# Kernel tuning notes

Hardware: AMD Instinct MI355X
Metric: run time of the kernel (lower is better)

Reference implementation:

```python
import jax, jax.numpy as jnp
import numpy as np

B, T, C = 1, 4096, 1024
H = 16
D = C // H  # 64
LN_EPS = 1e-5


def layer_norm(x, g, b):
    mu = jnp.mean(x, axis=-1, keepdims=True)
    var = jnp.mean(jnp.square(x - mu), axis=-1, keepdims=True)
    return (x - mu) * jax.lax.rsqrt(var + LN_EPS) * g + b


def setup_inputs() -> dict:
    key = jax.random.key(0)
    ks = jax.random.split(key, 8)
    s = 0.02
    return {
        "x": jax.random.normal(ks[0], (B, T, C), dtype=jnp.float32),
        "ln1_g": jnp.ones((C,), jnp.float32),
        "ln1_b": jnp.zeros((C,), jnp.float32),
        "Wqkv": jax.random.normal(ks[1], (C, 3 * C), dtype=jnp.float32) * s,
        "bqkv": jnp.zeros((3 * C,), jnp.float32),
        "Wo": jax.random.normal(ks[2], (C, C), dtype=jnp.float32) * s,
        "bo": jnp.zeros((C,), jnp.float32),
        "ln2_g": jnp.ones((C,), jnp.float32),
        "ln2_b": jnp.zeros((C,), jnp.float32),
        "W1": jax.random.normal(ks[3], (C, 4 * C), dtype=jnp.float32) * s,
        "b1": jnp.zeros((4 * C,), jnp.float32),
        "W2": jax.random.normal(ks[4], (4 * C, C), dtype=jnp.float32) * s,
        "b2": jnp.zeros((C,), jnp.float32),
    }


def reference(x, ln1_g, ln1_b, Wqkv, bqkv, Wo, bo, ln2_g, ln2_b, W1, b1, W2, b2):
    b, t, c = x.shape
    x_norm = layer_norm(x, ln1_g, ln1_b)
    qkv = x_norm @ Wqkv + bqkv                      # [B,T,3C]
    qkv = qkv.reshape(b, t, 3, H, D).transpose(2, 0, 3, 1, 4)  # [3,B,H,T,D]
    Q, K, V = qkv[0], qkv[1], qkv[2]
    scores = jnp.einsum("bhtd,bhsd->bhts", Q, K) / jnp.sqrt(jnp.float32(D))
    causal = jnp.tril(jnp.ones((t, t), dtype=bool))  # [T,T]
    scores = jnp.where(causal[None, None], scores, -jnp.inf)
    weights = jax.nn.softmax(scores, axis=-1)
    attn = jnp.einsum("bhts,bhsd->bhtd", weights, V)  # [B,H,T,D]
    attn = attn.transpose(0, 2, 1, 3).reshape(b, t, c)
    x = x + (attn @ Wo + bo)
    h = layer_norm(x, ln2_g, ln2_b)
    h = jax.nn.gelu(h @ W1 + b1, approximate=False) @ W2 + b2
    return x + h
```

## Files before the change

kernel.cpp:

```cpp
#include <hip/hip_runtime.h>
#include <math.h>

typedef __bf16 bf16_t;
typedef __attribute__((ext_vector_type(8))) __bf16 bf16x8;
typedef __attribute__((ext_vector_type(4))) __bf16 bf16x4;
typedef __attribute__((ext_vector_type(4))) float f32x4;
typedef __attribute__((ext_vector_type(16))) float f32x16;
typedef __attribute__((ext_vector_type(4))) unsigned int u32x4;

#define T_LEN 4096
#define C_DIM 1024
#define NH 16
#define HD 64

__device__ __forceinline__ void gload_lds16(const void* g, void* l) {
    __builtin_amdgcn_global_load_lds(
        (__attribute__((address_space(1))) void*)(g),
        (__attribute__((address_space(3))) void*)(l), 16, 0, 0);
}

__device__ __forceinline__ f32x4 mfma16(bf16x8 a, bf16x8 b, f32x4 c) {
    return __builtin_amdgcn_mfma_f32_16x16x32_bf16(a, b, c, 0, 0, 0);
}

__device__ __forceinline__ f32x16 mfma32(bf16x8 a, bf16x8 b, f32x16 c) {
    return __builtin_amdgcn_mfma_f32_32x32x16_bf16(a, b, c, 0, 0, 0);
}

__device__ __forceinline__ float gelu_exact(float v) {
    return 0.5f * v * (1.0f + erff(v * 0.7071067811865476f));
}

__device__ __forceinline__ void make_frags2(const f32x16 s, bf16x8& fx, bf16x8& fy) {
    unsigned a0, a1, b0, b1;
    asm("v_cvt_pk_bf16_f32 %0, %1, %2" : "=v"(a0) : "v"(s[0]), "v"(s[1]));
    asm("v_cvt_pk_bf16_f32 %0, %1, %2" : "=v"(a1) : "v"(s[2]), "v"(s[3]));
    asm("v_cvt_pk_bf16_f32 %0, %1, %2" : "=v"(b0) : "v"(s[4]), "v"(s[5]));
    asm("v_cvt_pk_bf16_f32 %0, %1, %2" : "=v"(b1) : "v"(s[6]), "v"(s[7]));
    asm("v_permlane32_swap_b32 %0, %1" : "+v"(a0), "+v"(b0));
    asm("v_permlane32_swap_b32 %0, %1" : "+v"(a1), "+v"(b1));
    u32x4 wa = {a0, a1, b0, b1};
    fx = __builtin_bit_cast(bf16x8, wa);
    unsigned c0, c1, d0, d1;
    asm("v_cvt_pk_bf16_f32 %0, %1, %2" : "=v"(c0) : "v"(s[8]), "v"(s[9]));
    asm("v_cvt_pk_bf16_f32 %0, %1, %2" : "=v"(c1) : "v"(s[10]), "v"(s[11]));
    asm("v_cvt_pk_bf16_f32 %0, %1, %2" : "=v"(d0) : "v"(s[12]), "v"(s[13]));
    asm("v_cvt_pk_bf16_f32 %0, %1, %2" : "=v"(d1) : "v"(s[14]), "v"(s[15]));
    asm("v_permlane32_swap_b32 %0, %1" : "+v"(c0), "+v"(d0));
    asm("v_permlane32_swap_b32 %0, %1" : "+v"(c1), "+v"(d1));
    u32x4 wb = {c0, c1, d0, d1};
    fy = __builtin_bit_cast(bf16x8, wb);
}

__global__ __launch_bounds__(256) void transpose_w(
    const float* __restrict__ in, bf16_t* __restrict__ out, int R, int C)
{
    __shared__ float tile[32][33];
    const int tx = threadIdx.x, ty = threadIdx.y;
    const int c0 = blockIdx.x * 32, r0 = blockIdx.y * 32;
#pragma unroll
    for (int j = 0; j < 4; ++j)
        tile[ty + j * 8][tx] = in[(size_t)(r0 + ty + j * 8) * C + c0 + tx];
    __syncthreads();
#pragma unroll
    for (int j = 0; j < 4; ++j)
        out[(size_t)(c0 + ty + j * 8) * R + r0 + tx] = (bf16_t)tile[tx][ty + j * 8];
}

__global__ __launch_bounds__(256) void vtrans(
    const bf16_t* __restrict__ qkv, bf16_t* __restrict__ vt)
{
    __shared__ bf16_t tile[32][33];
    const int tx = threadIdx.x, ty = threadIdx.y;
    const int h = blockIdx.z;
    const int t0 = blockIdx.x * 32, d0 = blockIdx.y * 32;
#pragma unroll
    for (int j = 0; j < 4; ++j)
        tile[ty + j * 8][tx] =
            qkv[(size_t)(t0 + ty + j * 8) * 3072 + 2048 + h * 64 + d0 + tx];
    __syncthreads();
#pragma unroll
    for (int j = 0; j < 4; ++j)
        vt[(size_t)h * (64 * 4096) + (size_t)(d0 + ty + j * 8) * 4096 + t0 + tx] =
            tile[tx][ty + j * 8];
}

__global__ __launch_bounds__(256) void ln_bf16(
    const float* __restrict__ x, const float* __restrict__ gam,
    const float* __restrict__ bet, bf16_t* __restrict__ out)
{
    const int row = blockIdx.x, t = threadIdx.x;
    const float4 v = *(const float4*)(x + (size_t)row * 1024 + t * 4);
    float s1 = v.x + v.y + v.z + v.w;
    float s2 = v.x * v.x + v.y * v.y + v.z * v.z + v.w * v.w;
#pragma unroll
    for (int m = 1; m < 64; m <<= 1) {
        s1 += __shfl_xor(s1, m);
        s2 += __shfl_xor(s2, m);
    }
    __shared__ float red[8];
    if ((t & 63) == 0) { red[(t >> 6) * 2] = s1; red[(t >> 6) * 2 + 1] = s2; }
    __syncthreads();
    s1 = red[0] + red[2] + red[4] + red[6];
    s2 = red[1] + red[3] + red[5] + red[7];
    const float mu = s1 * (1.0f / 1024.0f);
    const float inv = rsqrtf(s2 * (1.0f / 1024.0f) - mu * mu + 1e-5f);
    const float4 gg = *(const float4*)(gam + t * 4);
    const float4 bb = *(const float4*)(bet + t * 4);
    bf16x4 o;
    o[0] = (bf16_t)((v.x - mu) * inv * gg.x + bb.x);
    o[1] = (bf16_t)((v.y - mu) * inv * gg.y + bb.y);
    o[2] = (bf16_t)((v.z - mu) * inv * gg.z + bb.z);
    o[3] = (bf16_t)((v.w - mu) * inv * gg.w + bb.w);
    *(bf16x4*)(out + (size_t)row * 1024 + t * 4) = o;
}

template <int EPI>
__global__ __launch_bounds__(256, 2) void gemm_bt(
    const bf16_t* __restrict__ A, const bf16_t* __restrict__ Bt,
    const float* __restrict__ bias, const float* __restrict__ res,
    bf16_t* __restrict__ outb, float* __restrict__ outf,
    int M, int N, int K)
{
    __shared__ alignas(1024) bf16_t Alds[4][128 * 32];
    __shared__ alignas(1024) bf16_t Blds[4][128 * 32];
    const int t = threadIdx.x;
    const int lane = t & 63, w = t >> 6;
    const int wr = w >> 1, wc = w & 1;
    const int g = lane >> 4, ci = lane & 15;

    const int NB = gridDim.x, MB = gridDim.y;
    const int flat = blockIdx.x + NB * blockIdx.y;
    const int xcd = flat & 7, slot = flat >> 3;
    const int by = xcd * (MB >> 3) + slot / NB;
    const int bx = slot % NB;
    const int m0 = by * 128, n0 = bx * 128;

    f32x4 acc[4][4];
#pragma unroll
    for (int i = 0; i < 4; ++i)
#pragma unroll
        for (int j = 0; j < 4; ++j)
#pragma unroll
            for (int k = 0; k < 4; ++k) acc[i][j][k] = 0.0f;

    const int r0 = t >> 2;
    const int cc = (t & 3) * 8;
    const int nkt = K >> 5;

    auto stage = [&](int kt) {
        const int b = kt & 3;
        const int kk = kt * 32;
        char* aB = (char*)&Alds[b][0] + w * 1024;
        char* bB = (char*)&Blds[b][0] + w * 1024;
        gload_lds16(A + (size_t)(m0 + r0) * K + kk + cc, aB);
        gload_lds16(A + (size_t)(m0 + r0 + 64) * K + kk + cc, aB + 4096);
        gload_lds16(Bt + (size_t)(n0 + r0) * K + kk + cc, bB);
        gload_lds16(Bt + (size_t)(n0 + r0 + 64) * K + kk + cc, bB + 4096);
    };

    stage(0);
    if (nkt > 1) stage(1);
    for (int kt = 0; kt < nkt; ++kt) {
        if (kt + 2 < nkt) {
            stage(kt + 2);
            asm volatile("s_waitcnt vmcnt(8)" ::: "memory");
        } else if (kt + 1 < nkt) {
            asm volatile("s_waitcnt vmcnt(4)" ::: "memory");
        } else {
            asm volatile("s_waitcnt vmcnt(0)" ::: "memory");
        }
        __builtin_amdgcn_s_barrier();
        __builtin_amdgcn_sched_barrier(0);
        const int b = kt & 3;
        const bf16_t* ap = &Alds[b][0] + (wr * 64 + ci) * 32 + g * 8;
        const bf16_t* bp = &Blds[b][0] + (wc * 64 + ci) * 32 + g * 8;
        bf16x8 af[4], bf[4];
#pragma unroll
        for (int mt = 0; mt < 4; ++mt) af[mt] = *(const bf16x8*)(ap + mt * 16 * 32);
#pragma unroll
        for (int nt = 0; nt < 4; ++nt) bf[nt] = *(const bf16x8*)(bp + nt * 16 * 32);
        __builtin_amdgcn_s_setprio(1);
#pragma unroll
        for (int mt = 0; mt < 4; ++mt)
#pragma unroll
            for (int nt = 0; nt < 4; ++nt)
                acc[mt][nt] = mfma16(af[mt], bf[nt], acc[mt][nt]);
        __builtin_amdgcn_s_setprio(0);
    }

#pragma unroll
    for (int nt = 0; nt < 4; ++nt) {
        const int col = n0 + wc * 64 + nt * 16 + ci;
        const float bv = bias[col];
#pragma unroll
        for (int mt = 0; mt < 4; ++mt) {
            const int row = m0 + wr * 64 + mt * 16 + g * 4;
#pragma unroll
            for (int r = 0; r < 4; ++r) {
                float v = acc[mt][nt][r] + bv;
                if constexpr (EPI == 1) v = gelu_exact(v);
                if constexpr (EPI == 2) {
                    outf[(size_t)(row + r) * N + col] =
                        v + res[(size_t)(row + r) * N + col];
                } else {
                    outb[(size_t)(row + r) * N + col] = (bf16_t)v;
                }
            }
        }
    }
}

template <int EPI>
__global__ __launch_bounds__(512, 2) void gemm256(
    const bf16_t* __restrict__ A, const bf16_t* __restrict__ Bt,
    const float* __restrict__ bias, bf16_t* __restrict__ outb,
    int M, int N, int K)
{
    __shared__ alignas(1024) bf16_t lds[2][2][256 * 64];
    const int t = threadIdx.x, lane = t & 63, w = t >> 6;
    const int g = lane >> 4, ci = lane & 15;
    const int wr = w >> 2, wc = w & 3;
    const int m0 = blockIdx.y * 256, n0 = blockIdx.x * 256;
    const int NKT = K >> 6;

    f32x4 acc[8][4];
#pragma unroll
    for (int i = 0; i < 8; ++i)
#pragma unroll
        for (int j = 0; j < 4; ++j)
#pragma unroll
            for (int k2 = 0; k2 < 4; ++k2) acc[i][j][k2] = 0.0f;

    const int sw0 = (g ^ (ci & 7)) * 8;
    const int sw1 = ((4 + g) ^ (ci & 7)) * 8;

    auto stage = [&](int h, int ktile, int b) {
#pragma unroll
        for (int i = 0; i < 2; ++i) {
            const int idx = i * 512 + t;
            const int r = idx >> 3;
            const int c = (t & 7) ^ (r & 7);
            const bf16_t* src = ((h < 2) ? A : Bt)
                + (size_t)(((h < 2) ? m0 : n0) + (h & 1) * 128 + r) * K
                + ktile * 64 + c * 8;
            bf16_t* dst = &lds[b][h >> 1][(h & 1) * 8192] + (i * 512 + w * 64) * 8;
            gload_lds16(src, dst);
        }
    };

    bf16x8 a[4][2], b2[2][2][2];

    stage(0, 0, 0); stage(3, 0, 0); stage(1, 0, 0); stage(2, 0, 0);
    if (NKT > 1) { stage(0, 1, 1); stage(3, 1, 1); stage(1, 1, 1); }
    asm volatile("s_waitcnt vmcnt(6)" ::: "memory");
    __builtin_amdgcn_s_barrier();

    for (int kt = 0; kt < NKT; ++kt) {
        const int cur = kt & 1;
        const bf16_t* Ab = &lds[cur][0][0];
        const bf16_t* Bb = &lds[cur][1][0];

#pragma unroll
        for (int mi = 0; mi < 4; ++mi) {
            const bf16_t* ap = Ab + (wr * 64 + mi * 16 + ci) * 64;
            a[mi][0] = *(const bf16x8*)(ap + sw0);
            a[mi][1] = *(const bf16x8*)(ap + sw1);
        }
#pragma unroll
        for (int ni = 0; ni < 2; ++ni) {
            const bf16_t* bp = Bb + (wc * 32 + ni * 16 + ci) * 64;
            b2[0][ni][0] = *(const bf16x8*)(bp + sw0);
            b2[0][ni][1] = *(const bf16x8*)(bp + sw1);
        }
        if (kt + 1 < NKT) stage(2, kt + 1, cur ^ 1);
        __builtin_amdgcn_s_barrier();
        asm volatile("s_waitcnt lgkmcnt(0)" ::: "memory");
        __builtin_amdgcn_sched_barrier(0);
        __builtin_amdgcn_s_setprio(1);
#pragma unroll
        for (int mi = 0; mi < 4; ++mi)
#pragma unroll
            for (int ni = 0; ni < 2; ++ni) {
                acc[mi][ni] = mfma16(a[mi][0], b2[0][ni][0], acc[mi][ni]);
                acc[mi][ni] = mfma16(a[mi][1], b2[0][ni][1], acc[mi][ni]);
            }
        __builtin_amdgcn_s_setprio(0);
        __builtin_amdgcn_s_barrier();

#pragma unroll
        for (int ni = 0; ni < 2; ++ni) {
            const bf16_t* bp = Bb + (128 + wc * 32 + ni * 16 + ci) * 64;
            b2[1][ni][0] = *(const bf16x8*)(bp + sw0);
            b2[1][ni][1] = *(const bf16x8*)(bp + sw1);
        }
        if (kt + 2 < NKT) stage(0, kt + 2, cur);
        __builtin_amdgcn_s_barrier();
        asm volatile("s_waitcnt lgkmcnt(0)" ::: "memory");
        __builtin_amdgcn_sched_barrier(0);
        __builtin_amdgcn_s_setprio(1);
#pragma unroll
        for (int mi = 0; mi < 4; ++mi)
#pragma unroll
            for (int ni = 0; ni < 2; ++ni) {
                acc[mi][2 + ni] = mfma16(a[mi][0], b2[1][ni][0], acc[mi][2 + ni]);
                acc[mi][2 + ni] = mfma16(a[mi][1], b2[1][ni][1], acc[mi][2 + ni]);
            }
        __builtin_amdgcn_s_setprio(0);
        __builtin_amdgcn_s_barrier();

#pragma unroll
        for (int mi = 0; mi < 4; ++mi) {
            const bf16_t* ap = Ab + (128 + wr * 64 + mi * 16 + ci) * 64;
            a[mi][0] = *(const bf16x8*)(ap + sw0);
            a[mi][1] = *(const bf16x8*)(ap + sw1);
        }
        if (kt + 2 < NKT) stage(3, kt + 2, cur);
        __builtin_amdgcn_s_barrier();
        asm volatile("s_waitcnt lgkmcnt(0)" ::: "memory");
        __builtin_amdgcn_sched_barrier(0);
        __builtin_amdgcn_s_setprio(1);
#pragma unroll
        for (int mi = 0; mi < 4; ++mi)
#pragma unroll
            for (int ni = 0; ni < 2; ++ni) {
                acc[4 + mi][2 + ni] = mfma16(a[mi][0], b2[1][ni][0], acc[4 + mi][2 + ni]);
                acc[4 + mi][2 + ni] = mfma16(a[mi][1], b2[1][ni][1], acc[4 + mi][2 + ni]);
            }
        __builtin_amdgcn_s_setprio(0);
        __builtin_amdgcn_s_barrier();

        if (kt + 2 < NKT) stage(1, kt + 2, cur);
        __builtin_amdgcn_s_barrier();
        __builtin_amdgcn_s_setprio(1);
#pragma unroll
        for (int mi = 0; mi < 4; ++mi)
#pragma unroll
            for (int ni = 0; ni < 2; ++ni) {
                acc[4 + mi][ni] = mfma16(a[mi][0], b2[0][ni][0], acc[4 + mi][ni]);
                acc[4 + mi][ni] = mfma16(a[mi][1], b2[0][ni][1], acc[4 + mi][ni]);
            }
        __builtin_amdgcn_s_setprio(0);
        if (kt + 2 < NKT) asm volatile("s_waitcnt vmcnt(6)" ::: "memory");
        else              asm volatile("s_waitcnt vmcnt(0)" ::: "memory");
        __builtin_amdgcn_s_barrier();
    }

#pragma unroll
    for (int mrep = 0; mrep < 8; ++mrep) {
        const int row = m0 + (mrep >> 2) * 128 + wr * 64 + (mrep & 3) * 16 + g * 4;
#pragma unroll
        for (int nrep = 0; nrep < 4; ++nrep) {
            const int col = n0 + (nrep >> 1) * 128 + wc * 32 + (nrep & 1) * 16 + ci;
            const float bv = bias[col];
#pragma unroll
            for (int jr = 0; jr < 4; ++jr) {
                float v = acc[mrep][nrep][jr] + bv;
                if constexpr (EPI == 1) v = gelu_exact(v);
                outb[(size_t)(row + jr) * N + col] = (bf16_t)v;
            }
        }
    }
}

__global__ __launch_bounds__(256, 2) void attn_fwd(
    const bf16_t* __restrict__ qkv, const bf16_t* __restrict__ vt,
    float* __restrict__ opart, float* __restrict__ mlbuf)
{
    __shared__ alignas(1024) bf16_t Klds[2][64 * 64];
    __shared__ alignas(1024) bf16_t Vlds[2][64 * 64];
    const int t = threadIdx.x, lane = t & 63, w = t >> 6;
    const int hi = lane >> 5, li = lane & 31;
    const int lq = li >> 2;
    const int h = blockIdx.x;
    const int y = blockIdx.y;
    const int qt = 31 - (y >> 1);
    const int chunk = y & 1;
    const int q0 = qt * 128;
    const int qrow = q0 + w * 32 + li;
    const int wDiag = 2 * qt + (w >> 1);
    const int ktA = chunk ? (qt + 1) : 0;
    const int ktB = chunk ? (2 * qt + 2) : (qt + 1);
    const float C1 = 0.125f * 1.4426950408889634f;

    bf16x8 qf[4];
#pragma unroll
    for (int ks = 0; ks < 4; ++ks)
        qf[ks] = *(const bf16x8*)(qkv + (size_t)qrow * 3072 + h * 64 + ks * 16 + hi * 8);

    f32x16 oacc[2];
#pragma unroll
    for (int d = 0; d < 2; ++d)
#pragma unroll
        for (int r = 0; r < 16; ++r) oacc[d][r] = 0.0f;
    float m_i = -1e30f, l_i = 0.0f;

    const int sr = t >> 3;
    const int sx = ((t & 7) ^ ((sr >> 2) & 7)) * 8;

    auto stageKV = [&](int kt, int b) {
        const size_t kbase = (size_t)(kt * 64) * 3072 + 1024 + h * 64 + sx;
        const size_t vbase = (size_t)h * 262144 + (size_t)kt * 64 + sx;
#pragma unroll
        for (int i = 0; i < 2; ++i) {
            gload_lds16(qkv + kbase + (size_t)(i * 32 + sr) * 3072,
                        (char*)&Klds[b][0] + (size_t)(i * 2048 + t * 8) * 2);
            gload_lds16(vt + vbase + (size_t)(i * 32 + sr) * 4096,
                        (char*)&Vlds[b][0] + (size_t)(i * 2048 + t * 8) * 2);
        }
    };

    stageKV(ktA, 0);
    for (int kt = ktA; kt < ktB; ++kt) {
        const int cur = (kt - ktA) & 1;
        asm volatile("s_waitcnt vmcnt(0)" ::: "memory");
        __syncthreads();
        if (kt + 1 < ktB) stageKV(kt + 1, cur ^ 1);

        if (kt <= wDiag) {
            const bf16_t* Kb = &Klds[cur][0];
            const bf16_t* Vb = &Vlds[cur][0];
            f32x16 s0, s1;
#pragma unroll
            for (int r = 0; r < 16; ++r) { s0[r] = 0.0f; s1[r] = 0.0f; }

            __builtin_amdgcn_s_setprio(1);
#pragma unroll
            for (int ks = 0; ks < 4; ++ks) {
                const int cs = ((ks * 2 + hi) ^ lq) * 8;
                s0 = mfma32(*(const bf16x8*)(Kb + li * 64 + cs), qf[ks], s0);
                s1 = mfma32(*(const bf16x8*)(Kb + (32 + li) * 64 + cs), qf[ks], s1);
            }
            __builtin_amdgcn_s_setprio(0);

            bf16x8 vf[4][2];
#pragma unroll
            for (int ks = 0; ks < 4; ++ks) {
                const int cs = ((ks * 2 + hi) ^ lq) * 8;
                vf[ks][0] = *(const bf16x8*)(Vb + li * 64 + cs);
                vf[ks][1] = *(const bf16x8*)(Vb + (32 + li) * 64 + cs);
            }

            if (kt == wDiag) {
                const int kb0 = kt * 64 + 4 * hi;
#pragma unroll
                for (int r = 0; r < 16; ++r) {
                    const int kp0 = kb0 + (r & 3) + 8 * (r >> 2);
                    if (kp0 > qrow) s0[r] = -1e30f;
                    if (kp0 + 32 > qrow) s1[r] = -1e30f;
                }
            }
            float mt8[8];
#pragma unroll
            for (int r = 0; r < 8; ++r)
                mt8[r] = fmaxf(fmaxf(s0[r], s0[r + 8]), fmaxf(s1[r], s1[r + 8]));
#pragma unroll
            for (int d = 4; d >= 1; d >>= 1)
#pragma unroll
                for (int r = 0; r < d; ++r) mt8[r] = fmaxf(mt8[r], mt8[r + d]);
            float mx = fmaxf(mt8[0], __shfl_xor(mt8[0], 32));
            const float pmax = mx * C1;
            if (!__all(pmax - m_i <= 8.0f)) {
                const float newm = fmaxf(m_i, pmax);
                const float scf = exp2f(m_i - newm);
                m_i = newm;
                l_i *= scf;
#pragma unroll
                for (int r = 0; r < 16; ++r) { oacc[0][r] *= scf; oacc[1][r] *= scf; }
            }
            float st8[8];
#pragma unroll
            for (int r = 0; r < 16; ++r) {
                s0[r] = exp2f(fmaf(s0[r], C1, -m_i));
                s1[r] = exp2f(fmaf(s1[r], C1, -m_i));
            }
#pragma unroll
            for (int r = 0; r < 8; ++r)
                st8[r] = (s0[r] + s0[r + 8]) + (s1[r] + s1[r + 8]);
#pragma unroll
            for (int d = 4; d >= 1; d >>= 1)
#pragma unroll
                for (int r = 0; r < d; ++r) st8[r] += st8[r + d];
            l_i += st8[0] + __shfl_xor(st8[0], 32);

            bf16x8 pf[4];
            make_frags2(s0, pf[0], pf[1]);
            make_frags2(s1, pf[2], pf[3]);

            __builtin_amdgcn_s_setprio(1);
#pragma unroll
            for (int ks = 0; ks < 4; ++ks) {
                oacc[0] = mfma32(vf[ks][0], pf[ks], oacc[0]);
                oacc[1] = mfma32(vf[ks][1], pf[ks], oacc[1]);
            }
            __builtin_amdgcn_s_setprio(0);
        }
        __syncthreads();
    }

    float* op = opart + ((size_t)chunk * T_LEN + qrow) * 1024 + h * 64 + hi * 4;
#pragma unroll
    for (int dblk = 0; dblk < 2; ++dblk)
#pragma unroll
        for (int gi = 0; gi < 4; ++gi) {
            f32x4 o4;
#pragma unroll
            for (int j = 0; j < 4; ++j) o4[j] = oacc[dblk][gi * 4 + j];
            *(f32x4*)(op + dblk * 32 + gi * 8) = o4;
        }
    if (hi == 0) {
        float2 ml = make_float2(m_i, l_i);
        *(float2*)(mlbuf + (((size_t)chunk * T_LEN + qrow) * NH + h) * 2) = ml;
    }
}

__global__ __launch_bounds__(256) void attn_combine(
    const float* __restrict__ opart, const float* __restrict__ mlbuf,
    bf16_t* __restrict__ out)
{
    const int row = blockIdx.x, t = threadIdx.x;
    const int c = t * 4, h = c >> 6;
    const float2 ml0 = *(const float2*)(mlbuf + ((size_t)row * NH + h) * 2);
    const float2 ml1 = *(const float2*)(mlbuf + (((size_t)T_LEN + row) * NH + h) * 2);
    const float M = fmaxf(ml0.x, ml1.x);
    const float w0 = exp2f(ml0.x - M), w1 = exp2f(ml1.x - M);
    const float inv = 1.0f / (ml0.y * w0 + ml1.y * w1);
    const float4 o0 = *(const float4*)(opart + (size_t)row * 1024 + c);
    const float4 o1 = *(const float4*)(opart + ((size_t)T_LEN + row) * 1024 + c);
    bf16x4 o;
    o[0] = (bf16_t)((o0.x * w0 + o1.x * w1) * inv);
    o[1] = (bf16_t)((o0.y * w0 + o1.y * w1) * inv);
    o[2] = (bf16_t)((o0.z * w0 + o1.z * w1) * inv);
    o[3] = (bf16_t)((o0.w * w0 + o1.w * w1) * inv);
    *(bf16x4*)(out + (size_t)row * 1024 + c) = o;
}

extern "C" void kernel_launch(void* const* d_in, const int* in_sizes, int n_in,
                              void* d_out, int out_size, void* d_ws, size_t ws_size,
                              hipStream_t stream)
{
    const float* x    = (const float*)d_in[0];
    const float* ln1g = (const float*)d_in[1];
    const float* ln1b = (const float*)d_in[2];
    const float* Wqkv = (const float*)d_in[3];
    const float* bqkv = (const float*)d_in[4];
    const float* Wo   = (const float*)d_in[5];
    const float* bo   = (const float*)d_in[6];
    const float* ln2g = (const float*)d_in[7];
    const float* ln2b = (const float*)d_in[8];
    const float* W1   = (const float*)d_in[9];
    const float* b1   = (const float*)d_in[10];
    const float* W2   = (const float*)d_in[11];
    const float* b2   = (const float*)d_in[12];
    float* outp = (float*)d_out;

    char* p = (char*)d_ws;
    bf16_t* WqkvT = (bf16_t*)p; p += (size_t)3072 * 1024 * 2;
    bf16_t* WoT   = (bf16_t*)p; p += (size_t)1024 * 1024 * 2;
    bf16_t* W1T   = (bf16_t*)p; p += (size_t)4096 * 1024 * 2;
    bf16_t* W2T   = (bf16_t*)p; p += (size_t)1024 * 4096 * 2;
    bf16_t* xn    = (bf16_t*)p; p += (size_t)4096 * 1024 * 2;
    bf16_t* qkv   = (bf16_t*)p; p += (size_t)4096 * 3072 * 2;
    bf16_t* vtb   = (bf16_t*)p; p += (size_t)16 * 64 * 4096 * 2;
    bf16_t* attnb = (bf16_t*)p; p += (size_t)4096 * 1024 * 2;
    float*  x2    = (float*)p;  p += (size_t)4096 * 1024 * 4;
    bf16_t* hb    = (bf16_t*)p; p += (size_t)4096 * 1024 * 2;
    bf16_t* g1    = (bf16_t*)p; p += (size_t)4096 * 4096 * 2;
    float*  opart = (float*)p;  p += (size_t)2 * 4096 * 1024 * 4;
    float*  mlbuf = (float*)p;  p += (size_t)2 * 4096 * 16 * 2 * 4;

    const dim3 tb(32, 8);
    transpose_w<<<dim3(96, 32),  tb, 0, stream>>>(Wqkv, WqkvT, 1024, 3072);
    transpose_w<<<dim3(32, 32),  tb, 0, stream>>>(Wo,   WoT,   1024, 1024);
    transpose_w<<<dim3(128, 32), tb, 0, stream>>>(W1,   W1T,   1024, 4096);
    transpose_w<<<dim3(32, 128), tb, 0, stream>>>(W2,   W2T,   4096, 1024);

    ln_bf16<<<4096, 256, 0, stream>>>(x, ln1g, ln1b, xn);
    gemm256<0><<<dim3(12, 16), 512, 0, stream>>>(xn, WqkvT, bqkv,
                                                 qkv, 4096, 3072, 1024);
    vtrans<<<dim3(128, 2, 16), tb, 0, stream>>>(qkv, vtb);
    attn_fwd<<<dim3(16, 64), 256, 0, stream>>>(qkv, vtb, opart, mlbuf);
    attn_combine<<<4096, 256, 0, stream>>>(opart, mlbuf, attnb);
    gemm_bt<2><<<dim3(8, 32), 256, 0, stream>>>(attnb, WoT, bo, x,
                                                nullptr, x2, 4096, 1024, 1024);
    ln_bf16<<<4096, 256, 0, stream>>>(x2, ln2g, ln2b, hb);
    gemm256<1><<<dim3(16, 16), 512, 0, stream>>>(hb, W1T, b1,
                                                 g1, 4096, 4096, 1024);
    gemm_bt<2><<<dim3(8, 32), 256, 0, stream>>>(g1, W2T, b2, x2,
                                                nullptr, outp, 4096, 1024, 4096);
}
```

Before: 286.5 us.

## Split-K the W2 GEMM into two chunks and remap gemm256 tiles across XCDs

The final W2 GEMM (K=4096) is split into two K-halves, launched as 512 blocks instead of 256, each writing fp32 partials into the reused attention partial buffer. A new combine kernel sums both partials and adds the bias and the residual. This aims to fill more CUs, since 256 blocks of 128x128 tiles underfill the device, at the cost of extra fp32 partial traffic and one more launch. gemm256 also gets an XCD-aware block-index remap intended to improve L2 locality.

```diff
diff --git a/kernel.cpp b/kernel.cpp
--- a/kernel.cpp
+++ b/kernel.cpp
@@ -120,7 +120,7 @@
     const bf16_t* __restrict__ A, const bf16_t* __restrict__ Bt,
     const float* __restrict__ bias, const float* __restrict__ res,
     bf16_t* __restrict__ outb, float* __restrict__ outf,
-    int M, int N, int K)
+    int M, int N, int Klen, int Kstr)
 {
     __shared__ alignas(1024) bf16_t Alds[4][128 * 32];
     __shared__ alignas(1024) bf16_t Blds[4][128 * 32];
@@ -129,11 +129,23 @@
     const int wr = w >> 1, wc = w & 1;
     const int g = lane >> 4, ci = lane & 15;
 
-    const int NB = gridDim.x, MB = gridDim.y;
-    const int flat = blockIdx.x + NB * blockIdx.y;
-    const int xcd = flat & 7, slot = flat >> 3;
-    const int by = xcd * (MB >> 3) + slot / NB;
-    const int bx = slot % NB;
+    int bx, by, chunk = 0;
+    if constexpr (EPI == 3) {
+        const int flat = blockIdx.x + 8 * blockIdx.y;
+        const int xcd = flat & 7, s = flat >> 3;
+        chunk = s >> 5;
+        const int s2 = s & 31;
+        by = xcd * 4 + (s2 >> 3);
+        bx = s2 & 7;
+        A  += (size_t)chunk * Klen;
+        Bt += (size_t)chunk * Klen;
+    } else {
+        const int NB = gridDim.x, MB = gridDim.y;
+        const int flat = blockIdx.x + NB * blockIdx.y;
+        const int xcd = flat & 7, slot = flat >> 3;
+        by = xcd * (MB >> 3) + slot / NB;
+        bx = slot % NB;
+    }
     const int m0 = by * 128, n0 = bx * 128;
 
     f32x4 acc[4][4];
@@ -146,17 +158,17 @@
 
     const int r0 = t >> 2;
     const int cc = (t & 3) * 8;
-    const int nkt = K >> 5;
+    const int nkt = Klen >> 5;
 
     auto stage = [&](int kt) {
         const int b = kt & 3;
         const int kk = kt * 32;
         char* aB = (char*)&Alds[b][0] + w * 1024;
         char* bB = (char*)&Blds[b][0] + w * 1024;
-        gload_lds16(A + (size_t)(m0 + r0) * K + kk + cc, aB);
-        gload_lds16(A + (size_t)(m0 + r0 + 64) * K + kk + cc, aB + 4096);
-        gload_lds16(Bt + (size_t)(n0 + r0) * K + kk + cc, bB);
-        gload_lds16(Bt + (size_t)(n0 + r0 + 64) * K + kk + cc, bB + 4096);
+        gload_lds16(A + (size_t)(m0 + r0) * Kstr + kk + cc, aB);
+        gload_lds16(A + (size_t)(m0 + r0 + 64) * Kstr + kk + cc, aB + 4096);
+        gload_lds16(Bt + (size_t)(n0 + r0) * Kstr + kk + cc, bB);
+        gload_lds16(Bt + (size_t)(n0 + r0 + 64) * Kstr + kk + cc, bB + 4096);
     };
 
     stage(0);
@@ -192,7 +204,7 @@
 #pragma unroll
     for (int nt = 0; nt < 4; ++nt) {
         const int col = n0 + wc * 64 + nt * 16 + ci;
-        const float bv = bias[col];
+        const float bv = (EPI == 3) ? 0.0f : bias[col];
 #pragma unroll
         for (int mt = 0; mt < 4; ++mt) {
             const int row = m0 + wr * 64 + mt * 16 + g * 4;
@@ -203,12 +215,32 @@
                 if constexpr (EPI == 2) {
                     outf[(size_t)(row + r) * N + col] =
                         v + res[(size_t)(row + r) * N + col];
+                } else if constexpr (EPI == 3) {
+                    outf[((size_t)chunk * M + row + r) * N + col] = v;
                 } else {
                     outb[(size_t)(row + r) * N + col] = (bf16_t)v;
                 }
             }
         }
     }
+}
+
+__global__ __launch_bounds__(256) void w2_combine(
+    const float* __restrict__ part, const float* __restrict__ bias,
+    const float* __restrict__ res, float* __restrict__ out)
+{
+    const int row = blockIdx.x, t = threadIdx.x;
+    const int c = t * 4;
+    const float4 a = *(const float4*)(part + (size_t)row * 1024 + c);
+    const float4 b = *(const float4*)(part + ((size_t)T_LEN + row) * 1024 + c);
+    const float4 rr = *(const float4*)(res + (size_t)row * 1024 + c);
+    const float4 bb = *(const float4*)(bias + c);
+    float4 o;
+    o.x = a.x + b.x + rr.x + bb.x;
+    o.y = a.y + b.y + rr.y + bb.y;
+    o.z = a.z + b.z + rr.z + bb.z;
+    o.w = a.w + b.w + rr.w + bb.w;
+    *(float4*)(out + (size_t)row * 1024 + c) = o;
 }
 
 template <int EPI>
@@ -221,7 +253,11 @@
     const int t = threadIdx.x, lane = t & 63, w = t >> 6;
     const int g = lane >> 4, ci = lane & 15;
     const int wr = w >> 2, wc = w & 3;
-    const int m0 = blockIdx.y * 256, n0 = blockIdx.x * 256;
+    const int NB = gridDim.x;
+    const int nwg = NB * gridDim.y;
+    const int flat = blockIdx.x + NB * blockIdx.y;
+    const int rix = (flat & 7) * (nwg >> 3) + (flat >> 3);
+    const int m0 = (rix / NB) * 256, n0 = (rix % NB) * 256;
     const int NKT = K >> 6;
 
     f32x4 acc[8][4];
@@ -568,6 +604,7 @@
     bf16_t* g1    = (bf16_t*)p; p += (size_t)4096 * 4096 * 2;
     float*  opart = (float*)p;  p += (size_t)2 * 4096 * 1024 * 4;
     float*  mlbuf = (float*)p;  p += (size_t)2 * 4096 * 16 * 2 * 4;
+    float*  w2part = opart;
 
     const dim3 tb(32, 8);
     transpose_w<<<dim3(96, 32),  tb, 0, stream>>>(Wqkv, WqkvT, 1024, 3072);
@@ -582,10 +619,11 @@
     attn_fwd<<<dim3(16, 64), 256, 0, stream>>>(qkv, vtb, opart, mlbuf);
     attn_combine<<<4096, 256, 0, stream>>>(opart, mlbuf, attnb);
     gemm_bt<2><<<dim3(8, 32), 256, 0, stream>>>(attnb, WoT, bo, x,
-                                                nullptr, x2, 4096, 1024, 1024);
+                                                nullptr, x2, 4096, 1024, 1024, 1024);
     ln_bf16<<<4096, 256, 0, stream>>>(x2, ln2g, ln2b, hb);
     gemm256<1><<<dim3(16, 16), 512, 0, stream>>>(hb, W1T, b1,
                                                  g1, 4096, 4096, 1024);
-    gemm_bt<2><<<dim3(8, 32), 256, 0, stream>>>(g1, W2T, b2, x2,
-                                                nullptr, outp, 4096, 1024, 4096);
-}
+    gemm_bt<3><<<dim3(8, 64), 256, 0, stream>>>(g1, W2T, nullptr, nullptr,
+                                                nullptr, w2part, 4096, 1024, 2048, 4096);
+    w2_combine<<<4096, 256, 0, stream>>>(w2part, b2, x2, outp);
+}
```

Result: faster. 272.4 us (-4.9%).
